# Optimization experiments

Hardware: AMD Instinct MI355X
Metric: run time of the kernel (lower is better)

Reference implementation:

```python
import jax, jax.numpy as jnp
import numpy as np

NUM_LAYERS, D_IN, D_M, D_S, D_D, K = 4, 768, 1536, 16, 96, 4
EPS = 1e-6


def rmsnorm(x, w):
    return x * jax.lax.rsqrt(jnp.mean(x * x, axis=-1, keepdims=True) + EPS) * w


def depthwise_causal_conv(x, w, b):
    # x: [B, D_M, L], w: [D_M, K], b: [D_M]
    # torch Conv1d with padding=K-1 followed by [..., :L] == causal left-pad conv
    xp = jnp.pad(x, ((0, 0), (0, 0), (K - 1, 0)))
    y = jax.lax.conv_general_dilated(
        xp, w[:, None, :], (1,), 'VALID',
        dimension_numbers=('NCH', 'OIH', 'NCH'),
        feature_group_count=D_M)
    return y + b[None, :, None]


def mamba_block(seq, in_w, out_w, sB, sC, sD0, sD1w, sD1b, cw, cb, A_log, Dp):
    ab = seq @ in_w.T                       # [B,L,2*D_M]
    a, bgate = ab[..., :D_M], ab[..., D_M:]
    x = jnp.swapaxes(a, 1, 2)               # [B,D_M,L]
    a = jnp.swapaxes(depthwise_causal_conv(x, cw, cb), 1, 2)
    a = jax.nn.silu(a)
    # --- selective SSM ---
    A = -jnp.exp(A_log)                     # [D_M,D_S]
    Bm = a @ sB.T                           # [B,L,D_S]
    Cm = a @ sC.T                           # [B,L,D_S]
    delta = jax.nn.softplus((a @ sD0.T) @ sD1w.T + sD1b)  # [B,L,D_M]
    A_bar = jnp.exp(delta[..., None] * A)   # [B,L,D_M,D_S]
    X_bar = delta[..., None] * Bm[:, :, None, :] * a[..., None]

    def step(h, AX):
        At, Xt = AX                         # [B,D_M,D_S]
        h = At * h + Xt
        return h, h

    h0 = jnp.zeros((seq.shape[0], D_M, D_S), seq.dtype)
    _, hs = jax.lax.scan(step, h0, (jnp.swapaxes(A_bar, 0, 1), jnp.swapaxes(X_bar, 0, 1)))
    hid = jnp.swapaxes(hs, 0, 1)            # [B,L,D_M,D_S]
    out = jnp.einsum('blds,bls->bld', hid, Cm) + Dp * a
    out = out * jax.nn.silu(bgate)
    return out @ out_w.T


def setup_inputs() -> dict:
    key = jax.random.key(0)
    ks = jax.random.split(key, 16)
    s = 0.02
    tok = jax.random.randint(ks[0], (2, 1024), 0, 32000)
    embedding = jax.random.normal(ks[1], (32000, D_IN), jnp.float32) * s
    in_proj_w = jax.random.normal(ks[2], (NUM_LAYERS, 2 * D_M, D_IN), jnp.float32) * (D_IN ** -0.5)
    out_proj_w = jax.random.normal(ks[3], (NUM_LAYERS, D_IN, D_M), jnp.float32) * (D_M ** -0.5)
    sB_w = jax.random.normal(ks[4], (NUM_LAYERS, D_S, D_M), jnp.float32) * (D_M ** -0.5)
    sC_w = jax.random.normal(ks[5], (NUM_LAYERS, D_S, D_M), jnp.float32) * (D_M ** -0.5)
    sD0_w = jax.random.normal(ks[6], (NUM_LAYERS, D_D, D_M), jnp.float32) * (D_M ** -0.5)
    sD1_w = jax.random.uniform(ks[7], (NUM_LAYERS, D_M, D_D), jnp.float32, -(D_D ** -0.5), D_D ** -0.5)
    # dt-bias init exactly as in the module
    u = jax.random.uniform(ks[8], (NUM_LAYERS, D_M), jnp.float32)
    dt = jnp.clip(jnp.exp(u * (np.log(0.1) - np.log(0.001)) + np.log(0.001)), 1e-4, None)
    sD1_b = dt + jnp.log(-jnp.expm1(-dt))
    conv_w = jax.random.normal(ks[9], (NUM_LAYERS, D_M, K), jnp.float32) * (K ** -0.5)
    conv_b = jnp.zeros((NUM_LAYERS, D_M), jnp.float32)
    A_log = jnp.broadcast_to(jnp.log(jnp.arange(1, D_S + 1, dtype=jnp.float32)), (NUM_LAYERS, D_M, D_S))
    D = jnp.ones((NUM_LAYERS, D_M), jnp.float32)
    norm_w = jnp.ones((NUM_LAYERS, D_IN), jnp.float32)
    norm_f_w = jnp.ones((D_IN,), jnp.float32)
    head_w = jax.random.normal(ks[10], (32000, D_IN), jnp.float32) * (D_IN ** -0.5)
    return dict(tok=tok, embedding=embedding, in_proj_w=in_proj_w, out_proj_w=out_proj_w,
                sB_w=sB_w, sC_w=sC_w, sD0_w=sD0_w, sD1_w=sD1_w, sD1_b=sD1_b,
                conv_w=conv_w, conv_b=conv_b, A_log=A_log, D=D,
                norm_w=norm_w, norm_f_w=norm_f_w, head_w=head_w)


def reference(tok, embedding, in_proj_w, out_proj_w, sB_w, sC_w, sD0_w, sD1_w, sD1_b,
              conv_w, conv_b, A_log, D, norm_w, norm_f_w, head_w):
    seq = embedding[tok]                    # [B,L,D_IN]
    for i in range(NUM_LAYERS):
        seq = mamba_block(rmsnorm(seq, norm_w[i]),
                          in_proj_w[i], out_proj_w[i], sB_w[i], sC_w[i],
                          sD0_w[i], sD1_w[i], sD1_b[i], conv_w[i], conv_b[i],
                          A_log[i], D[i]) + seq
    seq = rmsnorm(seq, norm_f_w)
    return seq @ head_w.T                   # [B,L,vocab]
```

## Files before the change

kernel.cpp:

```cpp
#include <hip/hip_runtime.h>
#include <math.h>

#define BATCH 2
#define SEQLEN 1024
#define NTOK 2048
#define DIN 768
#define DM 1536
#define DS 16
#define DD 96
#define EPS 1e-6f
#define NC 64
#define CL 16
#define NG (BATCH*DM*DS)

typedef __attribute__((ext_vector_type(8))) short short8;
typedef __attribute__((ext_vector_type(4))) float f32x4;

static __device__ __forceinline__ unsigned short f2bf(float f) {
    unsigned int u = __float_as_uint(f);
    u += 0x7fff + ((u >> 16) & 1);
    return (unsigned short)(u >> 16);
}

__global__ __launch_bounds__(192) void embed_kernel(const int* __restrict__ tok,
                                                    const float* __restrict__ emb,
                                                    float* __restrict__ seq) {
    int m = blockIdx.x;
    int t = tok[m];
    const float4* src = (const float4*)(emb + (size_t)t * DIN);
    float4* dst = (float4*)(seq + (size_t)m * DIN);
    dst[threadIdx.x] = src[threadIdx.x];
}

__global__ __launch_bounds__(256) void zero_kernel(float* __restrict__ p, int n4) {
    int i = blockIdx.x * 256 + threadIdx.x;
    if (i < n4) ((float4*)p)[i] = make_float4(0.f, 0.f, 0.f, 0.f);
}

__global__ __launch_bounds__(256) void cast_kernel(const float* __restrict__ in,
                                                   unsigned short* __restrict__ out, int n4) {
    int i = blockIdx.x * 256 + threadIdx.x;
    if (i < n4) {
        float4 v = ((const float4*)in)[i];
        ushort4 r;
        r.x = f2bf(v.x); r.y = f2bf(v.y); r.z = f2bf(v.z); r.w = f2bf(v.w);
        ((ushort4*)out)[i] = r;
    }
}

__global__ __launch_bounds__(256) void wcat_kernel(const float* __restrict__ sB,
                                                   const float* __restrict__ sC,
                                                   const float* __restrict__ sD0,
                                                   unsigned short* __restrict__ out) {
    int idx = blockIdx.x * 256 + threadIdx.x;
    int k = idx % DM;
    int row = (idx / DM) & 127;
    int layer = idx / (DM * 128);
    float v;
    if (row < 16)      v = sB[((size_t)layer * 16 + row) * DM + k];
    else if (row < 32) v = sC[((size_t)layer * 16 + (row - 16)) * DM + k];
    else               v = sD0[((size_t)layer * 96 + (row - 32)) * DM + k];
    out[idx] = f2bf(v);
}

__global__ __launch_bounds__(256) void rmsnorm_kernel(const float* __restrict__ in,
                                                      const float* __restrict__ w,
                                                      unsigned short* __restrict__ out) {
    int m = blockIdx.x;
    const float* x = in + (size_t)m * DIN;
    float v[3];
    float s = 0.f;
#pragma unroll
    for (int j = 0; j < 3; j++) {
        v[j] = x[threadIdx.x + 256 * j];
        s += v[j] * v[j];
    }
#pragma unroll
    for (int off = 32; off; off >>= 1) s += __shfl_down(s, off);
    __shared__ float wsum[4];
    int lane = threadIdx.x & 63, wv = threadIdx.x >> 6;
    if (lane == 0) wsum[wv] = s;
    __syncthreads();
    float tot = wsum[0] + wsum[1] + wsum[2] + wsum[3];
    float scale = rsqrtf(tot / (float)DIN + EPS);
#pragma unroll
    for (int j = 0; j < 3; j++) {
        int c = threadIdx.x + 256 * j;
        out[(size_t)m * DIN + c] = f2bf(v[j] * scale * w[c]);
    }
}

template <int EPI, int KSPLIT, int XCDSWZ>
__global__ __launch_bounds__(256) void gemm_mfma(const unsigned short* __restrict__ A,
                                                 const unsigned short* __restrict__ B,
                                                 float* __restrict__ C, int N, int K, int nbx) {
    __shared__ unsigned short As[128 * 64];
    __shared__ unsigned short Bs[128 * 64];
    int tid = threadIdx.x;
    int lane = tid & 63, w = tid >> 6;
    int wm = w >> 1, wn = w & 1;
    int fm = lane & 15, fk = lane >> 4;

    int bx, by;
    if (XCDSWZ) {
        int lin = blockIdx.y * gridDim.x + blockIdx.x;
        int q = gridDim.x >> 3;
        int x = lin & 7;
        int t = lin >> 3;
        by = t % gridDim.y;
        bx = x * q + t / gridDim.y;
        if (bx >= nbx) return;
    } else {
        bx = blockIdx.x; by = blockIdx.y;
    }

    const unsigned short* Ab = A + (size_t)by * 128 * K;
    const unsigned short* Bb = B + (size_t)bx * 128 * K;

    int kchunk = K / KSPLIT;
    int kbeg = (KSPLIT > 1) ? blockIdx.z * kchunk : 0;
    int kend = kbeg + kchunk;

    int sr[4], so[4];
#pragma unroll
    for (int j = 0; j < 4; j++) {
        int c = tid + j * 256;
        int r = c >> 3;
        sr[j] = r;
        so[j] = ((c ^ r) & 7) * 8;
    }

    f32x4 acc[4][4];
#pragma unroll
    for (int i = 0; i < 4; i++)
#pragma unroll
        for (int j = 0; j < 4; j++) acc[i][j] = (f32x4){0.f, 0.f, 0.f, 0.f};

    for (int k0 = kbeg; k0 < kend; k0 += 64) {
        __syncthreads();
#pragma unroll
        for (int j = 0; j < 4; j++) {
            int c = tid + j * 256;
            __builtin_amdgcn_global_load_lds(
                (const __attribute__((address_space(1))) unsigned int*)(const void*)(Ab + (size_t)sr[j] * K + k0 + so[j]),
                (__attribute__((address_space(3))) unsigned int*)(void*)(As + c * 8), 16, 0, 0);
            __builtin_amdgcn_global_load_lds(
                (const __attribute__((address_space(1))) unsigned int*)(const void*)(Bb + (size_t)sr[j] * K + k0 + so[j]),
                (__attribute__((address_space(3))) unsigned int*)(void*)(Bs + c * 8), 16, 0, 0);
        }
        __syncthreads();

#pragma unroll
        for (int kk = 0; kk < 2; kk++) {
            short8 af[4], bfv[4];
#pragma unroll
            for (int i = 0; i < 4; i++) {
                int R = wm * 64 + i * 16 + fm;
                int dsw = (kk * 4 + fk) ^ (R & 7);
                af[i] = *(const short8*)(As + R * 64 + dsw * 8);
            }
#pragma unroll
            for (int j = 0; j < 4; j++) {
                int R = wn * 64 + j * 16 + fm;
                int dsw = (kk * 4 + fk) ^ (R & 7);
                bfv[j] = *(const short8*)(Bs + R * 64 + dsw * 8);
            }
#pragma unroll
            for (int i = 0; i < 4; i++)
#pragma unroll
                for (int j = 0; j < 4; j++)
                    acc[i][j] = __builtin_amdgcn_mfma_f32_16x16x32_bf16(af[i], bfv[j], acc[i][j], 0, 0, 0);
        }
    }

    int rowb = by * 128 + wm * 64;
    int colb = bx * 128 + wn * 64;
#pragma unroll
    for (int i = 0; i < 4; i++)
#pragma unroll
        for (int j = 0; j < 4; j++)
#pragma unroll
            for (int r = 0; r < 4; r++) {
                int row = rowb + i * 16 + fk * 4 + r;
                int col = colb + j * 16 + fm;
                size_t off = (size_t)row * N + col;
                if (EPI == 0)      C[off] = acc[i][j][r];
                else if (EPI == 1) C[off] += acc[i][j][r];
                else               unsafeAtomicAdd(&C[off], acc[i][j][r]);
            }
}

__global__ __launch_bounds__(256) void conv_silu_kernel(const float* __restrict__ ab,
                                                        const float* __restrict__ cw,
                                                        const float* __restrict__ cb,
                                                        float* __restrict__ out,
                                                        unsigned short* __restrict__ outb) {
    int idx = blockIdx.x * 256 + threadIdx.x;
    int c = idx % DM;
    int t = idx / DM;
    int l = t % SEQLEN;
    float4 w4 = ((const float4*)cw)[c];
    float y = cb[c];
    y = fmaf(w4.w, ab[(size_t)t * (2 * DM) + c], y);
    if (l >= 1) y = fmaf(w4.z, ab[(size_t)(t - 1) * (2 * DM) + c], y);
    if (l >= 2) y = fmaf(w4.y, ab[(size_t)(t - 2) * (2 * DM) + c], y);
    if (l >= 3) y = fmaf(w4.x, ab[(size_t)(t - 3) * (2 * DM) + c], y);
    float sv = y / (1.f + expf(-y));
    out[(size_t)t * DM + c] = sv;
    outb[(size_t)t * DM + c] = f2bf(sv);
}

__global__ __launch_bounds__(256) void gemm32_softplus(const float* __restrict__ A, int lda,
                                                       const float* __restrict__ B,
                                                       float* __restrict__ C, int N, int K,
                                                       const float* __restrict__ bias) {
    __shared__ float As[16][68];
    __shared__ float Bs[16][68];
    int tid = threadIdx.x;
    int lr = tid >> 2;
    int lk = (tid & 3) << 2;
    const float* Aptr = A + (size_t)(blockIdx.y * 64 + lr) * lda + lk;
    const float* Bptr = B + (size_t)(blockIdx.x * 64 + lr) * K + lk;
    int tx = tid & 15, ty = tid >> 4;
    float acc[4][4] = {};
    for (int k0 = 0; k0 < K; k0 += 16) {
        float4 av = *(const float4*)(Aptr + k0);
        float4 bv = *(const float4*)(Bptr + k0);
        __syncthreads();
        As[lk + 0][lr] = av.x; As[lk + 1][lr] = av.y;
        As[lk + 2][lr] = av.z; As[lk + 3][lr] = av.w;
        Bs[lk + 0][lr] = bv.x; Bs[lk + 1][lr] = bv.y;
        Bs[lk + 2][lr] = bv.z; Bs[lk + 3][lr] = bv.w;
        __syncthreads();
#pragma unroll
        for (int kk = 0; kk < 16; kk++) {
            float4 a4 = *(const float4*)&As[kk][ty * 4];
            float4 b4 = *(const float4*)&Bs[kk][tx * 4];
            float aa[4] = {a4.x, a4.y, a4.z, a4.w};
            float bb[4] = {b4.x, b4.y, b4.z, b4.w};
#pragma unroll
            for (int i = 0; i < 4; i++)
#pragma unroll
                for (int j = 0; j < 4; j++)
                    acc[i][j] = fmaf(aa[i], bb[j], acc[i][j]);
        }
    }
    int row0 = blockIdx.y * 64 + ty * 4;
    int col0 = blockIdx.x * 64 + tx * 4;
    float4 bsv = *(const float4*)(bias + col0);
    float bb[4] = {bsv.x, bsv.y, bsv.z, bsv.w};
#pragma unroll
    for (int i = 0; i < 4; i++) {
        float* cp = C + (size_t)(row0 + i) * N + col0;
        float r[4];
#pragma unroll
        for (int j = 0; j < 4; j++) {
            float xv = acc[i][j] + bb[j];
            r[j] = fmaxf(xv, 0.f) + log1pf(expf(-fabsf(xv)));
        }
        *(float4*)cp = make_float4(r[0], r[1], r[2], r[3]);
    }
}

__global__ __launch_bounds__(256) void scan_chunk(const float* __restrict__ delta,
                                                  const float* __restrict__ a,
                                                  const float* __restrict__ bcd,
                                                  const float* __restrict__ A_log,
                                                  float* __restrict__ P, float* __restrict__ S) {
    int tid = threadIdx.x;
    int blk = blockIdx.x;
    int dblk = blk % (DM / 256);
    int c = (blk / (DM / 256)) % NC;
    int b = blk / ((DM / 256) * NC);
    int d = dblk * 256 + tid;
    int t0 = b * SEQLEN + c * CL;

    __shared__ float LB[CL][16];
    {
        int row = tid >> 4, col = tid & 15;
        LB[row][col] = bcd[(size_t)(t0 + row) * 128 + col];
    }
    __syncthreads();

    float An[16];
    {
        const float4* ap = (const float4*)(A_log + (size_t)d * 16);
#pragma unroll
        for (int q = 0; q < 4; q++) {
            float4 v = ap[q];
            An[q * 4 + 0] = -expf(v.x); An[q * 4 + 1] = -expf(v.y);
            An[q * 4 + 2] = -expf(v.z); An[q * 4 + 3] = -expf(v.w);
        }
    }
    float h[16], Pv[16];
#pragma unroll
    for (int s = 0; s < 16; s++) { h[s] = 0.f; Pv[s] = 1.f; }

    for (int l = 0; l < CL; l++) {
        int t = t0 + l;
        float dv = delta[(size_t)t * DM + d];
        float av = a[(size_t)t * DM + d];
        float dva = dv * av;
#pragma unroll
        for (int s = 0; s < 16; s++) {
            float e = expf(dv * An[s]);
            Pv[s] *= e;
            h[s] = fmaf(e, h[s], dva * LB[l][s]);
        }
    }
    size_t g0 = (size_t)c * NG + (size_t)(b * DM + d) * 16;
#pragma unroll
    for (int q = 0; q < 4; q++) {
        *(f32x4*)(P + g0 + q * 4) = (f32x4){Pv[q*4], Pv[q*4+1], Pv[q*4+2], Pv[q*4+3]};
        *(f32x4*)(S + g0 + q * 4) = (f32x4){h[q*4], h[q*4+1], h[q*4+2], h[q*4+3]};
    }
}

__global__ __launch_bounds__(256) void scan_combine(const float* __restrict__ P,
                                                    const float* __restrict__ S,
                                                    float* __restrict__ Hb) {
    int g = blockIdx.x * 256 + threadIdx.x;
    float h = 0.f;
#pragma unroll
    for (int c = 0; c < NC; c++) {
        float Pv = P[c * NG + g];
        float Sv = S[c * NG + g];
        Hb[c * NG + g] = h;
        h = fmaf(Pv, h, Sv);
    }
}

__global__ __launch_bounds__(256) void scan_apply(const float* __restrict__ delta,
                                                  const float* __restrict__ a,
                                                  const float* __restrict__ bcd,
                                                  const float* __restrict__ ab,
                                                  const float* __restrict__ A_log,
                                                  const float* __restrict__ Dp,
                                                  const float* __restrict__ Hb,
                                                  unsigned short* __restrict__ y1b) {
    int tid = threadIdx.x;
    int blk = blockIdx.x;
    int dblk = blk % (DM / 256);
    int c = (blk / (DM / 256)) % NC;
    int b = blk / ((DM / 256) * NC);
    int d = dblk * 256 + tid;
    int t0 = b * SEQLEN + c * CL;

    __shared__ float LB[CL][32];
    {
        int row = tid >> 4, col = (tid & 15) * 2;
        *(float2*)&LB[row][col] = *(const float2*)&bcd[(size_t)(t0 + row) * 128 + col];
    }
    __syncthreads();

    float An[16];
    {
        const float4* ap = (const float4*)(A_log + (size_t)d * 16);
#pragma unroll
        for (int q = 0; q < 4; q++) {
            float4 v = ap[q];
            An[q * 4 + 0] = -expf(v.x); An[q * 4 + 1] = -expf(v.y);
            An[q * 4 + 2] = -expf(v.z); An[q * 4 + 3] = -expf(v.w);
        }
    }
    float Dv = Dp[d];
    float h[16];
    {
        const float* hp = Hb + (size_t)c * NG + (size_t)(b * DM + d) * 16;
#pragma unroll
        for (int q = 0; q < 4; q++) {
            float4 v = *(const float4*)(hp + q * 4);
            h[q * 4 + 0] = v.x; h[q * 4 + 1] = v.y; h[q * 4 + 2] = v.z; h[q * 4 + 3] = v.w;
        }
    }

    for (int l = 0; l < CL; l++) {
        int t = t0 + l;
        float dv = delta[(size_t)t * DM + d];
        float av = a[(size_t)t * DM + d];
        float dva = dv * av;
        float ct = 0.f;
#pragma unroll
        for (int s = 0; s < 16; s++) {
            float e = expf(dv * An[s]);
            h[s] = fmaf(e, h[s], dva * LB[l][s]);
            ct = fmaf(h[s], LB[l][16 + s], ct);
        }
        float bg = ab[(size_t)t * 2 * DM + DM + d];
        float sl = bg / (1.f + expf(-bg));
        float y = (ct + Dv * av) * sl;
        y1b[(size_t)t * DM + d] = f2bf(y);
    }
}

extern "C" void kernel_launch(void* const* d_in, const int* in_sizes, int n_in,
                              void* d_out, int out_size, void* d_ws, size_t ws_size,
                              hipStream_t stream) {
    const int* tok        = (const int*)d_in[0];
    const float* emb      = (const float*)d_in[1];
    const float* in_proj  = (const float*)d_in[2];
    const float* out_proj = (const float*)d_in[3];
    const float* sB       = (const float*)d_in[4];
    const float* sC       = (const float*)d_in[5];
    const float* sD0      = (const float*)d_in[6];
    const float* sD1      = (const float*)d_in[7];
    const float* sD1b     = (const float*)d_in[8];
    const float* cw       = (const float*)d_in[9];
    const float* cb       = (const float*)d_in[10];
    const float* A_log    = (const float*)d_in[11];
    const float* Dp       = (const float*)d_in[12];
    const float* norm_w   = (const float*)d_in[13];
    const float* norm_f   = (const float*)d_in[14];
    const float* head_w   = (const float*)d_in[15];
    float* out = (float*)d_out;

    char* base = (char*)d_ws;
    float* seq   = (float*)base;          base += (size_t)NTOK * DIN * 4;
    float* ab    = (float*)base;          base += (size_t)NTOK * 2 * DM * 4;
    float* ac    = (float*)base;          base += (size_t)NTOK * DM * 4;
    float* delta = (float*)base;          base += (size_t)NTOK * DM * 4;
    float* bcd   = (float*)base;          base += (size_t)NTOK * 128 * 4;
    unsigned short* xnb  = (unsigned short*)base;  base += (size_t)NTOK * DIN * 2;
    unsigned short* acb  = (unsigned short*)base;  base += (size_t)NTOK * DM * 2;
    unsigned short* y1b  = (unsigned short*)base;  base += (size_t)NTOK * DM * 2;
    float* P  = (float*)base;             base += (size_t)NG * NC * 4;
    float* S  = (float*)base;             base += (size_t)NG * NC * 4;
    unsigned short* inpb  = (unsigned short*)base; base += (size_t)4 * 2 * DM * DIN * 2;
    unsigned short* outpb = (unsigned short*)base; base += (size_t)4 * DIN * DM * 2;
    unsigned short* wcatb = (unsigned short*)base; base += (size_t)4 * 128 * DM * 2;
    float* Hb = P;
    unsigned short* headb = (unsigned short*)ab;

    embed_kernel<<<NTOK, 192, 0, stream>>>(tok, emb, seq);
    wcat_kernel<<<4 * 128 * DM / 256, 256, 0, stream>>>(sB, sC, sD0, wcatb);
    cast_kernel<<<(4 * 2 * DM * DIN / 4 + 255) / 256, 256, 0, stream>>>(in_proj, inpb, 4 * 2 * DM * DIN / 4);
    cast_kernel<<<(4 * DIN * DM / 4 + 255) / 256, 256, 0, stream>>>(out_proj, outpb, 4 * DIN * DM / 4);

    for (int i = 0; i < 4; i++) {
        rmsnorm_kernel<<<NTOK, 256, 0, stream>>>(seq, norm_w + i * DIN, xnb);
        gemm_mfma<0, 1, 1><<<dim3(2 * DM / 128, NTOK / 128), 256, 0, stream>>>(
            xnb, inpb + (size_t)i * 2 * DM * DIN, ab, 2 * DM, DIN, 2 * DM / 128);
        conv_silu_kernel<<<NTOK * DM / 256, 256, 0, stream>>>(
            ab, cw + (size_t)i * DM * 4, cb + (size_t)i * DM, ac, acb);
        zero_kernel<<<NTOK * 128 / 4 / 256, 256, 0, stream>>>(bcd, NTOK * 128 / 4);
        gemm_mfma<2, 8, 0><<<dim3(1, NTOK / 128, 8), 256, 0, stream>>>(
            acb, wcatb + (size_t)i * 128 * DM, bcd, 128, DM, 1);
        gemm32_softplus<<<dim3(DM / 64, NTOK / 64), 256, 0, stream>>>(
            bcd + 32, 128, sD1 + (size_t)i * DM * DD, delta, DM, DD, sD1b + (size_t)i * DM);
        scan_chunk<<<BATCH * NC * (DM / 256), 256, 0, stream>>>(
            delta, ac, bcd, A_log + (size_t)i * DM * DS, P, S);
        scan_combine<<<NG / 256, 256, 0, stream>>>(P, S, Hb);
        scan_apply<<<BATCH * NC * (DM / 256), 256, 0, stream>>>(
            delta, ac, bcd, ab, A_log + (size_t)i * DM * DS, Dp + (size_t)i * DM, Hb, y1b);
        gemm_mfma<2, 4, 0><<<dim3(DIN / 128, NTOK / 128, 4), 256, 0, stream>>>(
            y1b, outpb + (size_t)i * DIN * DM, seq, DIN, DM, DIN / 128);
    }
    rmsnorm_kernel<<<NTOK, 256, 0, stream>>>(seq, norm_f, xnb);
    cast_kernel<<<(32000 * DIN / 4 + 255) / 256, 256, 0, stream>>>(head_w, headb, 32000 * DIN / 4);
    gemm_mfma<0, 1, 1><<<dim3(256, NTOK / 128), 256, 0, stream>>>(
        xnb, headb, out, 32000, DIN, 32000 / 128);
}
```

Before: 1.309 ms.

## Double-buffer GEMM LDS tiles with 32-wide K steps and prefetch

Splits the 128x64 LDS tiles into two 128x32 buffers and prefetches the next K-slice with global_load_lds while MFMAs run on the current one. This drops one barrier per iteration and aims to overlap global loads with compute. It adds a new swizzle that packs two rows per 64-element LDS line and sets a minimum occupancy of 4 blocks via launch bounds. The shorter K step per barrier and the possible register pressure from that occupancy hint could offset the gain.

Measured after the change: 1.290 ms. Within noise of the previous version (-1.5%).

```diff
diff --git a/kernel.cpp b/kernel.cpp
--- a/kernel.cpp
+++ b/kernel.cpp
@@ -91,11 +91,11 @@
 }
 
 template <int EPI, int KSPLIT, int XCDSWZ>
-__global__ __launch_bounds__(256) void gemm_mfma(const unsigned short* __restrict__ A,
-                                                 const unsigned short* __restrict__ B,
-                                                 float* __restrict__ C, int N, int K, int nbx) {
-    __shared__ unsigned short As[128 * 64];
-    __shared__ unsigned short Bs[128 * 64];
+__global__ __launch_bounds__(256, 4) void gemm_mfma(const unsigned short* __restrict__ A,
+                                                    const unsigned short* __restrict__ B,
+                                                    float* __restrict__ C, int N, int K, int nbx) {
+    __shared__ unsigned short As[2][128 * 32];
+    __shared__ unsigned short Bs[2][128 * 32];
     int tid = threadIdx.x;
     int lane = tid & 63, w = tid >> 6;
     int wm = w >> 1, wn = w & 1;
@@ -119,15 +119,25 @@
 
     int kchunk = K / KSPLIT;
     int kbeg = (KSPLIT > 1) ? blockIdx.z * kchunk : 0;
-    int kend = kbeg + kchunk;
-
-    int sr[4], so[4];
-#pragma unroll
-    for (int j = 0; j < 4; j++) {
+    int nt = kchunk >> 5;
+
+    int srcR[2], srcO[2];
+#pragma unroll
+    for (int j = 0; j < 2; j++) {
         int c = tid + j * 256;
-        int r = c >> 3;
-        sr[j] = r;
-        so[j] = ((c ^ r) & 7) * 8;
+        int p = c >> 3;
+        int u = (c & 7) ^ (p & 7);
+        srcR[j] = p * 2 + (u >> 2);
+        srcO[j] = (u & 3) * 8;
+    }
+
+    int aoff[4], boff[4];
+#pragma unroll
+    for (int i = 0; i < 4; i++) {
+        int R = wm * 64 + i * 16 + fm;
+        aoff[i] = (R >> 1) * 64 + (((((R & 1) << 2) | fk) ^ ((R >> 1) & 7)) * 8);
+        int Rb = wn * 64 + i * 16 + fm;
+        boff[i] = (Rb >> 1) * 64 + (((((Rb & 1) << 2) | fk) ^ ((Rb >> 1) & 7)) * 8);
     }
 
     f32x4 acc[4][4];
@@ -136,41 +146,36 @@
 #pragma unroll
         for (int j = 0; j < 4; j++) acc[i][j] = (f32x4){0.f, 0.f, 0.f, 0.f};
 
-    for (int k0 = kbeg; k0 < kend; k0 += 64) {
-        __syncthreads();
-#pragma unroll
-        for (int j = 0; j < 4; j++) {
+    auto STAGE = [&](int buf, int k0) {
+#pragma unroll
+        for (int j = 0; j < 2; j++) {
             int c = tid + j * 256;
             __builtin_amdgcn_global_load_lds(
-                (const __attribute__((address_space(1))) unsigned int*)(const void*)(Ab + (size_t)sr[j] * K + k0 + so[j]),
-                (__attribute__((address_space(3))) unsigned int*)(void*)(As + c * 8), 16, 0, 0);
+                (const __attribute__((address_space(1))) unsigned int*)(const void*)(Ab + (size_t)srcR[j] * K + k0 + srcO[j]),
+                (__attribute__((address_space(3))) unsigned int*)(void*)(&As[buf][0] + c * 8), 16, 0, 0);
             __builtin_amdgcn_global_load_lds(
-                (const __attribute__((address_space(1))) unsigned int*)(const void*)(Bb + (size_t)sr[j] * K + k0 + so[j]),
-                (__attribute__((address_space(3))) unsigned int*)(void*)(Bs + c * 8), 16, 0, 0);
-        }
+                (const __attribute__((address_space(1))) unsigned int*)(const void*)(Bb + (size_t)srcR[j] * K + k0 + srcO[j]),
+                (__attribute__((address_space(3))) unsigned int*)(void*)(&Bs[buf][0] + c * 8), 16, 0, 0);
+        }
+    };
+
+    STAGE(0, kbeg);
+    __syncthreads();
+    int cur = 0;
+    for (int t = 0; t < nt; ++t) {
+        if (t + 1 < nt) STAGE(cur ^ 1, kbeg + (t + 1) * 32);
+        short8 af[4], bfv[4];
+#pragma unroll
+        for (int i = 0; i < 4; i++) af[i] = *(const short8*)(&As[cur][0] + aoff[i]);
+#pragma unroll
+        for (int j = 0; j < 4; j++) bfv[j] = *(const short8*)(&Bs[cur][0] + boff[j]);
+#pragma unroll
+        for (int i = 0; i < 4; i++)
+#pragma unroll
+            for (int j = 0; j < 4; j++)
+                acc[i][j] = __builtin_amdgcn_mfma_f32_16x16x32_bf16(af[i], bfv[j], acc[i][j], 0, 0, 0);
         __syncthreads();
-
-#pragma unroll
-        for (int kk = 0; kk < 2; kk++) {
-            short8 af[4], bfv[4];
-#pragma unroll
-            for (int i = 0; i < 4; i++) {
-                int R = wm * 64 + i * 16 + fm;
-                int dsw = (kk * 4 + fk) ^ (R & 7);
-                af[i] = *(const short8*)(As + R * 64 + dsw * 8);
-            }
-#pragma unroll
-            for (int j = 0; j < 4; j++) {
-                int R = wn * 64 + j * 16 + fm;
-                int dsw = (kk * 4 + fk) ^ (R & 7);
-                bfv[j] = *(const short8*)(Bs + R * 64 + dsw * 8);
-            }
-#pragma unroll
-            for (int i = 0; i < 4; i++)
-#pragma unroll
-                for (int j = 0; j < 4; j++)
-                    acc[i][j] = __builtin_amdgcn_mfma_f32_16x16x32_bf16(af[i], bfv[j], acc[i][j], 0, 0, 0);
-        }
+        cur ^= 1;
     }
 
     int rowb = by * 128 + wm * 64;
```
